# Kernel tuning notes

Hardware: AMD Instinct MI355X
Metric: run time of the kernel (lower is better)

## Reference

```python
import jax, jax.numpy as jnp
import numpy as np

B, N, D, H = 4, 2048, 1024, 16
DH = D // H  # head dim = 64


def positional_encoding(n, dim):
    # Faithful vectorization of the numpy double loop in PositionalEncoding.
    i = jnp.arange(dim)
    even_i = (i % 2) == 0
    denom_i = 10000.0 ** (2.0 * jnp.where(even_i, i, i - 1).astype(jnp.float32) / dim)
    pos = jnp.arange(n, dtype=jnp.float32)[:, None]  # [n,1]
    base = jnp.where(even_i[None, :], jnp.sin(pos / denom_i), jnp.cos(pos / denom_i))  # [n,dim]
    p = jnp.arange(n)
    even_p = (p % 2) == 0
    denom_p = 10000.0 ** (2.0 * jnp.where(even_p, p, p - 1).astype(jnp.float32) / n)  # [n]
    j = jnp.arange(dim, dtype=jnp.float32)[None, :]  # [1,dim]
    mult = jnp.where(even_p[:, None], jnp.sin(j / denom_p[:, None]), jnp.cos(j / denom_p[:, None]))  # [n,dim]
    return base * mult


def setup_inputs() -> dict:
    key = jax.random.key(0)
    ks = jax.random.split(key, 4)
    s = 1.0 / np.sqrt(D)
    return {
        "data": jax.random.normal(ks[0], (B, N, D), dtype=jnp.float32),
        "Wq": jax.random.normal(ks[1], (D, D), dtype=jnp.float32) * s,
        "bq": jnp.zeros((D,), dtype=jnp.float32),
        "Wk": jax.random.normal(ks[2], (D, D), dtype=jnp.float32) * s,
        "bk": jnp.zeros((D,), dtype=jnp.float32),
        "Wv": jax.random.normal(ks[3], (D, D), dtype=jnp.float32) * s,
        "bv": jnp.zeros((D,), dtype=jnp.float32),
    }


def _split_heads(x):
    # tf.concat(tf.split(x, H, axis=-1), axis=0): head-major [H*B, N, DH]
    b, n, d = x.shape
    return x.reshape(b, n, H, DH).transpose(2, 0, 1, 3).reshape(H * b, n, DH)


def reference(data, Wq, bq, Wk, bk, Wv, bv):
    b, n, d = data.shape
    x = data + positional_encoding(n, d).astype(data.dtype)  # [B,N,D]
    q = _split_heads(x @ Wq + bq)  # [H*B,N,DH]
    k = _split_heads(x @ Wk + bk)
    v = _split_heads(x @ Wv + bv)
    # scale uses last dim of key AFTER split, i.e. head_dim
    scores = jnp.einsum('bqd,bkd->bqk', q, k) / jnp.sqrt(jnp.float32(DH))  # [H*B,N,N]
    w = jax.nn.softmax(scores, axis=-1)
    return jnp.einsum('bqk,bkd->bqd', w, v)  # [H*B,N,DH]
```

## Files before the change

### kernel.cpp

```cpp
#include <hip/hip_runtime.h>
#include <hip/hip_bf16.h>

#define BB 4
#define NN 2048
#define DD 1024
#define HH 16
#define DHH 64
#define HB (HH*BB)

typedef __bf16 bf16;
typedef __bf16 bf16x4v __attribute__((ext_vector_type(4)));
typedef __bf16 bf16x8 __attribute__((ext_vector_type(8)));
typedef float f32x4 __attribute__((ext_vector_type(4)));
typedef float f32x16 __attribute__((ext_vector_type(16)));
typedef unsigned u32x2 __attribute__((ext_vector_type(2)));

#if __has_builtin(__builtin_amdgcn_permlane32_swap)
#define HAVE_PLSWAP 1
#else
#define HAVE_PLSWAP 0
#endif

#define QSCALE 0.18033688011112042f

__device__ __forceinline__ void async16(const void* g, void* l) {
    __builtin_amdgcn_global_load_lds(
        (const __attribute__((address_space(1))) unsigned int*)g,
        (__attribute__((address_space(3))) unsigned int*)l, 16, 0, 0);
}

__device__ __forceinline__ unsigned pkbf(float a, float b) {
    union { bf16 h[2]; unsigned u; } x;
    x.h[0] = (bf16)a; x.h[1] = (bf16)b;
    return x.u;
}

__global__ void pe_add_kernel(const float* __restrict__ data, bf16* __restrict__ xb) {
    int t = blockIdx.x * blockDim.x + threadIdx.x;
    int base = t * 4;
    int row = base >> 10;
    int d0 = base & 1023;
    int n = row & (NN - 1);
    const float LOG2_10000 = 13.287712379549449f;
    int pn = n & ~1;
    float denom_p = __builtin_amdgcn_exp2f((2.0f * (float)pn / (float)NN) * LOG2_10000);
    bool even_p = (n & 1) == 0;
    float4 dv = *(const float4*)(data + base);
    float din[4] = {dv.x, dv.y, dv.z, dv.w};
    bf16x4v ov;
    #pragma unroll
    for (int u = 0; u < 4; ++u) {
        int d = d0 + u;
        int di = d & ~1;
        float denom_i = __builtin_amdgcn_exp2f((2.0f * (float)di / (float)DD) * LOG2_10000);
        float a = (float)n / denom_i;
        float basev = ((d & 1) == 0) ? __sinf(a) : __cosf(a);
        float bm = (float)d / denom_p;
        float mult = even_p ? __sinf(bm) : __cosf(bm);
        ov[u] = (bf16)(din[u] + basev * mult);
    }
    *(bf16x4v*)(xb + base) = ov;
}

__global__ void wtrans_kernel(const float* __restrict__ Wq, const float* __restrict__ Wk,
                              const float* __restrict__ Wv, bf16* __restrict__ Bw) {
    const float* W = (blockIdx.z == 0) ? Wq : (blockIdx.z == 1) ? Wk : Wv;
    bf16* Wt = Bw + (size_t)blockIdx.z * 1024 * 1024;
    __shared__ float s[32][33];
    int bx = blockIdx.x * 32;
    int by = blockIdx.y * 32;
    int tx = threadIdx.x, ty = threadIdx.y;
    #pragma unroll
    for (int i = 0; i < 32; i += 8)
        s[ty + i][tx] = W[(by + ty + i) * DD + bx + tx];
    __syncthreads();
    #pragma unroll
    for (int i = 0; i < 32; i += 8)
        Wt[(size_t)(bx + ty + i) * DD + by + tx] = (bf16)s[tx][ty + i];
}

__launch_bounds__(256)
__global__ void gemm_qkv_fused(const bf16* __restrict__ A,
                               const bf16* __restrict__ Bw,
                               const float* __restrict__ bq, const float* __restrict__ bk,
                               const float* __restrict__ bv,
                               bf16* __restrict__ Qs, bf16* __restrict__ Ks,
                               bf16* __restrict__ Vb) {
    __shared__ char smem[36864];
    int tid = threadIdx.x;
    int w = tid >> 6, lane = tid & 63, l32 = lane & 31, hi = lane >> 5;
    int bi = blockIdx.x;
    int bn = bi >> 6;
    int bm = (bi & 7) * 8 + ((bi >> 3) & 7);
    int m0 = bm * 128, n0 = bn * 128;
    int wm = (w & 1) * 64, wn = (w >> 1) * 64;

    int srow = tid >> 2;
    int g4 = (tid & 3) ^ (srow & 3);
    const bf16* aS0 = A + (size_t)(m0 + srow) * DD + g4 * 8;
    const bf16* aS1 = aS0 + (size_t)64 * DD;
    const bf16* bS0 = Bw + (size_t)(n0 + srow) * DD + g4 * 8;
    const bf16* bS1 = bS0 + (size_t)64 * DD;

    f32x16 acc[2][2];
    #pragma unroll
    for (int i = 0; i < 2; ++i)
        #pragma unroll
        for (int j = 0; j < 2; ++j)
            #pragma unroll
            for (int r = 0; r < 16; ++r) acc[i][j][r] = 0.f;

    async16(aS0, smem + w * 1024);
    async16(aS1, smem + 4096 + w * 1024);
    async16(bS0, smem + 8192 + w * 1024);
    async16(bS1, smem + 12288 + w * 1024);
    __syncthreads();

    for (int kk = 0; kk < DD; kk += 32) {
        char* buf  = smem + ((kk >> 5) & 1) * 16384;
        char* nbuf = smem + (((kk >> 5) & 1) ^ 1) * 16384;
        if (kk + 32 < DD) {
            async16(aS0 + kk + 32, nbuf + w * 1024);
            async16(aS1 + kk + 32, nbuf + 4096 + w * 1024);
            async16(bS0 + kk + 32, nbuf + 8192 + w * 1024);
            async16(bS1 + kk + 32, nbuf + 12288 + w * 1024);
        }
        const char* As = buf;
        const char* Bs = buf + 8192;
        bf16x8 af[2][2], bfr[2][2];
        #pragma unroll
        for (int mt = 0; mt < 2; ++mt) {
            int row = wm + mt * 32 + l32;
            #pragma unroll
            for (int kc = 0; kc < 2; ++kc)
                af[mt][kc] = *(const bf16x8*)(As + row * 64 + ((kc * 2 + hi) ^ (l32 & 3)) * 16);
        }
        #pragma unroll
        for (int nt = 0; nt < 2; ++nt) {
            int row = wn + nt * 32 + l32;
            #pragma unroll
            for (int kc = 0; kc < 2; ++kc)
                bfr[nt][kc] = *(const bf16x8*)(Bs + row * 64 + ((kc * 2 + hi) ^ (l32 & 3)) * 16);
        }
        #pragma unroll
        for (int mt = 0; mt < 2; ++mt)
            #pragma unroll
            for (int nt = 0; nt < 2; ++nt)
                #pragma unroll
                for (int kc = 0; kc < 2; ++kc)
                    acc[mt][nt] = __builtin_amdgcn_mfma_f32_32x32x16_bf16(
                        af[mt][kc], bfr[nt][kc], acc[mt][nt], 0, 0, 0);
        __syncthreads();
    }

    int mat = n0 >> 10;
    if (mat < 2) {
        const float* bias_p = (mat == 0) ? bq : bk;
        #pragma unroll
        for (int nt = 0; nt < 2; ++nt) {
            int ncol = (n0 + wn + nt * 32 + l32) & 1023;
            float bias = bias_p[ncol];
            int h = ncol >> 6, dh = ncol & 63;
            #pragma unroll
            for (int mt = 0; mt < 2; ++mt) {
                int rowbase = m0 + wm + mt * 32 + 4 * hi;
                #pragma unroll
                for (int m4 = 0; m4 < 4; ++m4) {
                    #pragma unroll
                    for (int rr = 0; rr < 4; ++rr) {
                        int mrow = rowbase + 8 * m4 + rr;
                        int b_ = mrow >> 11, nn_ = mrow & 2047;
                        int hbi = h * BB + b_;
                        float v = acc[mt][nt][m4 * 4 + rr] + bias;
                        if (mat == 0)
                            Qs[((size_t)hbi * NN + nn_) * DHH + dh] = (bf16)(v * QSCALE);
                        else
                            Ks[((size_t)hbi * NN + nn_) * DHH + dh] = (bf16)v;
                    }
                }
            }
        }
    } else {
        bf16* vl = (bf16*)smem;
        #pragma unroll
        for (int nt = 0; nt < 2; ++nt) {
            int ncol_l = wn + nt * 32 + l32;
            float bias = bv[(n0 + ncol_l) & 1023];
            #pragma unroll
            for (int mt = 0; mt < 2; ++mt) {
                int m_base = wm + mt * 32 + 4 * hi;
                #pragma unroll
                for (int m4 = 0; m4 < 4; ++m4) {
                    bf16x4v q;
                    #pragma unroll
                    for (int rr = 0; rr < 4; ++rr)
                        q[rr] = (bf16)(acc[mt][nt][m4 * 4 + rr] + bias);
                    *(bf16x4v*)(vl + ncol_l * 130 + m_base + 8 * m4) = q;
                }
            }
        }
        __syncthreads();
        int b_ = m0 >> 11, nn0 = m0 & 2047;
        #pragma unroll
        for (int p = 0; p < 2; ++p) {
            int ncol = p * 64 + (tid >> 2);
            int ncg = (n0 + ncol) & 1023;
            int h = ncg >> 6, dh = ncg & 63;
            bf16* dst = Vb + ((size_t)(h * BB + b_) * DHH + dh) * NN + nn0;
            #pragma unroll
            for (int i = 0; i < 4; ++i) {
                int eoff = ((tid & 3) + 4 * i) * 8;
                bf16x8 vv = *(const bf16x8*)(vl + ncol * 130 + eoff);
                *(bf16x8*)(dst + eoff) = vv;
            }
        }
    }
}

__launch_bounds__(256, 3)
__global__ void attn_kernel(const bf16* __restrict__ Qs,
                            const bf16* __restrict__ Ks,
                            const bf16* __restrict__ Vb,
                            float* __restrict__ out) {
    __shared__ char smem[49664];
    int tid = threadIdx.x;
    int w = tid >> 6, lane = tid & 63, l32 = lane & 31, hi = lane >> 5;
    int qh = w & 1, kh = w >> 1;
    int bi = blockIdx.x;
    int xcd = bi & 7, jj = bi >> 3;
    int hb = xcd * 8 + (jj & 7);
    int qb = jj >> 3;
    int q0 = qb * 128;

    bf16x8 qf[2][4];
    #pragma unroll
    for (int qs = 0; qs < 2; ++qs) {
        const bf16* qbase = Qs + ((size_t)hb * NN + q0 + qh * 64 + qs * 32 + l32) * DHH + hi * 8;
        #pragma unroll
        for (int c = 0; c < 4; ++c)
            qf[qs][c] = *(const bf16x8*)(qbase + c * 16);
    }

    int srow = tid >> 3;
    int g8 = (tid & 7) ^ (srow & 7);
    const bf16* ksrc = Ks + ((size_t)hb * NN + srow) * DHH + g8 * 8;
    const bf16* vsrc = Vb + ((size_t)hb * DHH + srow) * NN + g8 * 8;

    f32x16 o[2][2];
    #pragma unroll
    for (int qs = 0; qs < 2; ++qs)
        #pragma unroll
        for (int d = 0; d < 2; ++d)
            #pragma unroll
            for (int r = 0; r < 16; ++r) o[qs][d][r] = 0.f;
    float ts[2] = {0.f, 0.f};

    {
        char* b0 = smem;
        char* b1 = smem + 16384;
        async16(ksrc,                      b0 + w * 1024);
        async16(ksrc + 32 * 64,            b0 + 4096 + w * 1024);
        async16(vsrc,                      b0 + 8192 + w * 1024);
        async16(vsrc + (size_t)32 * NN,    b0 + 12288 + w * 1024);
        async16(ksrc + 64 * 64,            b1 + w * 1024);
        async16(ksrc + 96 * 64,            b1 + 4096 + w * 1024);
        async16(vsrc + 64,                 b1 + 8192 + w * 1024);
        async16(vsrc + (size_t)32 * NN + 64, b1 + 12288 + w * 1024);
    }
    asm volatile("s_waitcnt vmcnt(4)" ::: "memory");
    __builtin_amdgcn_s_barrier();

    int bsel = 0;
    for (int kt = 0; kt < NN; kt += 64) {
        char* buf = smem + bsel * 16384;
        bool pf = (kt + 128) < NN;
        if (pf) {
            int pb = bsel + 2; if (pb >= 3) pb -= 3;
            char* nbuf = smem + pb * 16384;
            async16(ksrc + (size_t)(kt + 128) * 64,      nbuf + w * 1024);
            async16(ksrc + (size_t)(kt + 160) * 64,      nbuf + 4096 + w * 1024);
            async16(vsrc + (kt + 128),                   nbuf + 8192 + w * 1024);
            async16(vsrc + (size_t)32 * NN + (kt + 128), nbuf + 12288 + w * 1024);
        }
        const char* ktile = buf;
        const char* vtile = buf + 8192;

        bf16x8 kf[4];
        int krow = kh * 32 + l32;
        #pragma unroll
        for (int c = 0; c < 4; ++c)
            kf[c] = *(const bf16x8*)(ktile + krow * 128 + ((c * 2 + hi) ^ (l32 & 7)) * 16);

        f32x16 sa[2];
        #pragma unroll
        for (int qs = 0; qs < 2; ++qs) {
            #pragma unroll
            for (int r = 0; r < 16; ++r) sa[qs][r] = 0.f;
            #pragma unroll
            for (int c = 0; c < 4; ++c)
                sa[qs] = __builtin_amdgcn_mfma_f32_32x32x16_bf16(kf[c], qf[qs][c], sa[qs], 0, 0, 0);
        }

        unsigned dw[2][4][2];
        #pragma unroll
        for (int qs = 0; qs < 2; ++qs) {
            float t0 = 0.f;
            #pragma unroll
            for (int m4 = 0; m4 < 4; ++m4) {
                float p0 = __builtin_amdgcn_exp2f(sa[qs][m4 * 4 + 0]);
                float p1 = __builtin_amdgcn_exp2f(sa[qs][m4 * 4 + 1]);
                float p2 = __builtin_amdgcn_exp2f(sa[qs][m4 * 4 + 2]);
                float p3 = __builtin_amdgcn_exp2f(sa[qs][m4 * 4 + 3]);
                t0 += (p0 + p1) + (p2 + p3);
                dw[qs][m4][0] = pkbf(p0, p1);
                dw[qs][m4][1] = pkbf(p2, p3);
            }
            ts[qs] += t0;
        }

        #pragma unroll
        for (int kc = 0; kc < 2; ++kc) {
            bf16x8 vf[2];
            #pragma unroll
            for (int d = 0; d < 2; ++d) {
                int vrow = d * 32 + l32;
                vf[d] = *(const bf16x8*)(vtile + vrow * 128 +
                                         ((kh * 4 + kc * 2 + hi) ^ (l32 & 7)) * 16);
            }
            #pragma unroll
            for (int qs = 0; qs < 2; ++qs) {
                int mlo = kc * 2;
                unsigned a0 = dw[qs][mlo][0],     a1 = dw[qs][mlo][1];
                unsigned b0 = dw[qs][mlo + 1][0], b1 = dw[qs][mlo + 1][1];
                union { unsigned u[4]; bf16x8 v; } pu;
#if HAVE_PLSWAP
                u32x2 r0 = __builtin_amdgcn_permlane32_swap(a0, b0, false, false);
                u32x2 r1 = __builtin_amdgcn_permlane32_swap(a1, b1, false, false);
                pu.u[0] = r0.x; pu.u[1] = r1.x; pu.u[2] = r0.y; pu.u[3] = r1.y;
#else
                unsigned own0 = hi ? b0 : a0, own1 = hi ? b1 : a1;
                unsigned snd0 = hi ? a0 : b0, snd1 = hi ? a1 : b1;
                unsigned rcv0 = __shfl_xor(snd0, 32, 64);
                unsigned rcv1 = __shfl_xor(snd1, 32, 64);
                pu.u[0] = hi ? rcv0 : own0;
                pu.u[1] = hi ? rcv1 : own1;
                pu.u[2] = hi ? own0 : rcv0;
                pu.u[3] = hi ? own1 : rcv1;
#endif
                #pragma unroll
                for (int d = 0; d < 2; ++d)
                    o[qs][d] = __builtin_amdgcn_mfma_f32_32x32x16_bf16(vf[d], pu.v, o[qs][d], 0, 0, 0);
            }
        }

        if (pf) asm volatile("s_waitcnt vmcnt(4)" ::: "memory");
        else    asm volatile("s_waitcnt vmcnt(0)" ::: "memory");
        __builtin_amdgcn_s_barrier();
        bsel = bsel + 1; if (bsel >= 3) bsel = 0;
    }
    __syncthreads();

    float* Osm = (float*)smem;
    float* Ls  = (float*)(smem + 49152);
    float tsq[2];
    #pragma unroll
    for (int qs = 0; qs < 2; ++qs)
        tsq[qs] = ts[qs] + __shfl_xor(ts[qs], 32, 64);

    if (kh == 0) {
        #pragma unroll
        for (int qs = 0; qs < 2; ++qs) {
            int q_l = qh * 64 + qs * 32 + l32;
            #pragma unroll
            for (int d = 0; d < 2; ++d)
                #pragma unroll
                for (int m4 = 0; m4 < 4; ++m4) {
                    int ci = d * 8 + m4 * 2 + hi;
                    int pc = ci ^ (q_l & 15);
                    f32x4 v;
                    v[0] = o[qs][d][m4 * 4 + 0];
                    v[1] = o[qs][d][m4 * 4 + 1];
                    v[2] = o[qs][d][m4 * 4 + 2];
                    v[3] = o[qs][d][m4 * 4 + 3];
                    *(f32x4*)(Osm + q_l * 64 + pc * 4) = v;
                }
            if (!hi) Ls[q_l] = tsq[qs];
        }
    }
    __syncthreads();
    if (kh == 1) {
        #pragma unroll
        for (int qs = 0; qs < 2; ++qs) {
            int q_l = qh * 64 + qs * 32 + l32;
            #pragma unroll
            for (int d = 0; d < 2; ++d)
                #pragma unroll
                for (int m4 = 0; m4 < 4; ++m4) {
                    int ci = d * 8 + m4 * 2 + hi;
                    int pc = ci ^ (q_l & 15);
                    f32x4 v = *(const f32x4*)(Osm + q_l * 64 + pc * 4);
                    v[0] += o[qs][d][m4 * 4 + 0];
                    v[1] += o[qs][d][m4 * 4 + 1];
                    v[2] += o[qs][d][m4 * 4 + 2];
                    v[3] += o[qs][d][m4 * 4 + 3];
                    *(f32x4*)(Osm + q_l * 64 + pc * 4) = v;
                }
            if (!hi) Ls[q_l] += tsq[qs];
        }
    }
    __syncthreads();
    float* outb = out + ((size_t)hb * NN + q0) * DHH;
    #pragma unroll
    for (int i = 0; i < 8; ++i) {
        int g = tid + 256 * i;
        int q_l = g >> 4, ci = g & 15;
        int pc = ci ^ (q_l & 15);
        float inv = 1.0f / Ls[q_l];
        f32x4 v = *(const f32x4*)(Osm + q_l * 64 + pc * 4);
        v *= inv;
        *(f32x4*)(outb + g * 4) = v;
    }
}

extern "C" void kernel_launch(void* const* d_in, const int* in_sizes, int n_in,
                              void* d_out, int out_size, void* d_ws, size_t ws_size,
                              hipStream_t stream) {
    const float* data = (const float*)d_in[0];
    const float* Wq   = (const float*)d_in[1];
    const float* bq   = (const float*)d_in[2];
    const float* Wk   = (const float*)d_in[3];
    const float* bk   = (const float*)d_in[4];
    const float* Wv   = (const float*)d_in[5];
    const float* bv   = (const float*)d_in[6];
    float* out = (float*)d_out;

    char* ws = (char*)d_ws;
    bf16* xb = (bf16*)ws; ws += (size_t)8192 * 1024 * 2;
    bf16* Bw = (bf16*)ws; ws += (size_t)3072 * 1024 * 2;
    bf16* Qs = (bf16*)ws; ws += (size_t)HB * NN * DHH * 2;
    bf16* Ks = (bf16*)ws; ws += (size_t)HB * NN * DHH * 2;
    bf16* Vb = (bf16*)ws; ws += (size_t)HB * NN * DHH * 2;

    pe_add_kernel<<<8192, 256, 0, stream>>>(data, xb);
    dim3 tb(32, 8), tg(32, 32, 3);
    wtrans_kernel<<<tg, tb, 0, stream>>>(Wq, Wk, Wv, Bw);
    gemm_qkv_fused<<<1536, 256, 0, stream>>>(xb, Bw, bq, bk, bv, Qs, Ks, Vb);
    attn_kernel<<<1024, 256, 0, stream>>>(Qs, Ks, Vb, out);
}
```

Before: 248.2 us.

## Double attention query tile to 256 with 8 waves and merge prep kernels

The attention kernel now runs 512-thread blocks (4 query-halves × 2 key-halves of waves) covering 256 queries per block. Each block loads each K/V tile once for twice as many queries, which halves global K/V traffic per query, and each thread now issues a single async load per tile. The positional-encoding add and the weight transpose/convert are merged into one launch to save one kernel launch. The costs are a larger LDS footprint, fewer blocks (512) over the CUs, and a launch-bounds hint of 4 waves per EU that could cap registers below what the previous setting allowed and force spills.

```diff
diff --git a/kernel.cpp b/kernel.cpp
--- a/kernel.cpp
+++ b/kernel.cpp
@@ -35,48 +35,55 @@
     return x.u;
 }
 
-__global__ void pe_add_kernel(const float* __restrict__ data, bf16* __restrict__ xb) {
-    int t = blockIdx.x * blockDim.x + threadIdx.x;
-    int base = t * 4;
-    int row = base >> 10;
-    int d0 = base & 1023;
-    int n = row & (NN - 1);
-    const float LOG2_10000 = 13.287712379549449f;
-    int pn = n & ~1;
-    float denom_p = __builtin_amdgcn_exp2f((2.0f * (float)pn / (float)NN) * LOG2_10000);
-    bool even_p = (n & 1) == 0;
-    float4 dv = *(const float4*)(data + base);
-    float din[4] = {dv.x, dv.y, dv.z, dv.w};
-    bf16x4v ov;
-    #pragma unroll
-    for (int u = 0; u < 4; ++u) {
-        int d = d0 + u;
-        int di = d & ~1;
-        float denom_i = __builtin_amdgcn_exp2f((2.0f * (float)di / (float)DD) * LOG2_10000);
-        float a = (float)n / denom_i;
-        float basev = ((d & 1) == 0) ? __sinf(a) : __cosf(a);
-        float bm = (float)d / denom_p;
-        float mult = even_p ? __sinf(bm) : __cosf(bm);
-        ov[u] = (bf16)(din[u] + basev * mult);
-    }
-    *(bf16x4v*)(xb + base) = ov;
-}
-
-__global__ void wtrans_kernel(const float* __restrict__ Wq, const float* __restrict__ Wk,
-                              const float* __restrict__ Wv, bf16* __restrict__ Bw) {
-    const float* W = (blockIdx.z == 0) ? Wq : (blockIdx.z == 1) ? Wk : Wv;
-    bf16* Wt = Bw + (size_t)blockIdx.z * 1024 * 1024;
+__global__ void pe_wtrans_kernel(const float* __restrict__ data,
+                                 const float* __restrict__ Wq, const float* __restrict__ Wk,
+                                 const float* __restrict__ Wv,
+                                 bf16* __restrict__ xb, bf16* __restrict__ Bw) {
     __shared__ float s[32][33];
-    int bx = blockIdx.x * 32;
-    int by = blockIdx.y * 32;
-    int tx = threadIdx.x, ty = threadIdx.y;
-    #pragma unroll
-    for (int i = 0; i < 32; i += 8)
-        s[ty + i][tx] = W[(by + ty + i) * DD + bx + tx];
-    __syncthreads();
-    #pragma unroll
-    for (int i = 0; i < 32; i += 8)
-        Wt[(size_t)(bx + ty + i) * DD + by + tx] = (bf16)s[tx][ty + i];
+    int b = blockIdx.x;
+    int tid = threadIdx.x;
+    if (b < 8192) {
+        int t = b * 256 + tid;
+        int base = t * 4;
+        int row = base >> 10;
+        int d0 = base & 1023;
+        int n = row & (NN - 1);
+        const float LOG2_10000 = 13.287712379549449f;
+        int pn = n & ~1;
+        float denom_p = __builtin_amdgcn_exp2f((2.0f * (float)pn / (float)NN) * LOG2_10000);
+        bool even_p = (n & 1) == 0;
+        float4 dv = *(const float4*)(data + base);
+        float din[4] = {dv.x, dv.y, dv.z, dv.w};
+        bf16x4v ov;
+        #pragma unroll
+        for (int u = 0; u < 4; ++u) {
+            int d = d0 + u;
+            int di = d & ~1;
+            float denom_i = __builtin_amdgcn_exp2f((2.0f * (float)di / (float)DD) * LOG2_10000);
+            float a = (float)n / denom_i;
+            float basev = ((d & 1) == 0) ? __sinf(a) : __cosf(a);
+            float bm = (float)d / denom_p;
+            float mult = even_p ? __sinf(bm) : __cosf(bm);
+            ov[u] = (bf16)(din[u] + basev * mult);
+        }
+        *(bf16x4v*)(xb + base) = ov;
+    } else {
+        int bb = b - 8192;
+        int bz = bb >> 10;
+        int rem = bb & 1023;
+        int by = (rem >> 5) * 32;
+        int bx = (rem & 31) * 32;
+        const float* W = (bz == 0) ? Wq : (bz == 1) ? Wk : Wv;
+        bf16* Wt = Bw + (size_t)bz * 1024 * 1024;
+        int tx = tid & 31, ty = tid >> 5;
+        #pragma unroll
+        for (int i = 0; i < 32; i += 8)
+            s[ty + i][tx] = W[(by + ty + i) * DD + bx + tx];
+        __syncthreads();
+        #pragma unroll
+        for (int i = 0; i < 32; i += 8)
+            Wt[(size_t)(bx + ty + i) * DD + by + tx] = (bf16)s[tx][ty + i];
+    }
 }
 
 __launch_bounds__(256)
@@ -217,20 +224,20 @@
     }
 }
 
-__launch_bounds__(256, 3)
+__launch_bounds__(512, 4)
 __global__ void attn_kernel(const bf16* __restrict__ Qs,
                             const bf16* __restrict__ Ks,
                             const bf16* __restrict__ Vb,
                             float* __restrict__ out) {
-    __shared__ char smem[49664];
+    __shared__ char smem[66560];
     int tid = threadIdx.x;
     int w = tid >> 6, lane = tid & 63, l32 = lane & 31, hi = lane >> 5;
-    int qh = w & 1, kh = w >> 1;
+    int qh = w & 3, kh = w >> 2;
     int bi = blockIdx.x;
     int xcd = bi & 7, jj = bi >> 3;
     int hb = xcd * 8 + (jj & 7);
     int qb = jj >> 3;
-    int q0 = qb * 128;
+    int q0 = qb * 256;
 
     bf16x8 qf[2][4];
     #pragma unroll
@@ -258,16 +265,12 @@
     {
         char* b0 = smem;
         char* b1 = smem + 16384;
-        async16(ksrc,                      b0 + w * 1024);
-        async16(ksrc + 32 * 64,            b0 + 4096 + w * 1024);
-        async16(vsrc,                      b0 + 8192 + w * 1024);
-        async16(vsrc + (size_t)32 * NN,    b0 + 12288 + w * 1024);
-        async16(ksrc + 64 * 64,            b1 + w * 1024);
-        async16(ksrc + 96 * 64,            b1 + 4096 + w * 1024);
-        async16(vsrc + 64,                 b1 + 8192 + w * 1024);
-        async16(vsrc + (size_t)32 * NN + 64, b1 + 12288 + w * 1024);
-    }
-    asm volatile("s_waitcnt vmcnt(4)" ::: "memory");
+        async16(ksrc,           b0 + w * 1024);
+        async16(vsrc,           b0 + 8192 + w * 1024);
+        async16(ksrc + 64 * 64, b1 + w * 1024);
+        async16(vsrc + 64,      b1 + 8192 + w * 1024);
+    }
+    asm volatile("s_waitcnt vmcnt(2)" ::: "memory");
     __builtin_amdgcn_s_barrier();
 
     int bsel = 0;
@@ -277,10 +280,8 @@
         if (pf) {
             int pb = bsel + 2; if (pb >= 3) pb -= 3;
             char* nbuf = smem + pb * 16384;
-            async16(ksrc + (size_t)(kt + 128) * 64,      nbuf + w * 1024);
-            async16(ksrc + (size_t)(kt + 160) * 64,      nbuf + 4096 + w * 1024);
-            async16(vsrc + (kt + 128),                   nbuf + 8192 + w * 1024);
-            async16(vsrc + (size_t)32 * NN + (kt + 128), nbuf + 12288 + w * 1024);
+            async16(ksrc + (size_t)(kt + 128) * 64, nbuf + w * 1024);
+            async16(vsrc + (kt + 128),              nbuf + 8192 + w * 1024);
         }
         const char* ktile = buf;
         const char* vtile = buf + 8192;
@@ -353,7 +354,7 @@
             }
         }
 
-        if (pf) asm volatile("s_waitcnt vmcnt(4)" ::: "memory");
+        if (pf) asm volatile("s_waitcnt vmcnt(2)" ::: "memory");
         else    asm volatile("s_waitcnt vmcnt(0)" ::: "memory");
         __builtin_amdgcn_s_barrier();
         bsel = bsel + 1; if (bsel >= 3) bsel = 0;
@@ -361,7 +362,7 @@
     __syncthreads();
 
     float* Osm = (float*)smem;
-    float* Ls  = (float*)(smem + 49152);
+    float* Ls  = (float*)(smem + 65536);
     float tsq[2];
     #pragma unroll
     for (int qs = 0; qs < 2; ++qs)
@@ -412,7 +413,7 @@
     float* outb = out + ((size_t)hb * NN + q0) * DHH;
     #pragma unroll
     for (int i = 0; i < 8; ++i) {
-        int g = tid + 256 * i;
+        int g = tid + 512 * i;
         int q_l = g >> 4, ci = g & 15;
         int pc = ci ^ (q_l & 15);
         float inv = 1.0f / Ls[q_l];
@@ -441,9 +442,7 @@
     bf16* Ks = (bf16*)ws; ws += (size_t)HB * NN * DHH * 2;
     bf16* Vb = (bf16*)ws; ws += (size_t)HB * NN * DHH * 2;
 
-    pe_add_kernel<<<8192, 256, 0, stream>>>(data, xb);
-    dim3 tb(32, 8), tg(32, 32, 3);
-    wtrans_kernel<<<tg, tb, 0, stream>>>(Wq, Wk, Wv, Bw);
+    pe_wtrans_kernel<<<11264, 256, 0, stream>>>(data, Wq, Wk, Wv, xb, Bw);
     gemm_qkv_fused<<<1536, 256, 0, stream>>>(xb, Bw, bq, bk, bv, Qs, Ks, Vb);
-    attn_kernel<<<1024, 256, 0, stream>>>(Qs, Ks, Vb, out);
-}
+    attn_kernel<<<512, 512, 0, stream>>>(Qs, Ks, Vb, out);
+}
```

New measurement: 509.7 us. 2.05x slower.
